# Optimization experiments

Measured on AMD Instinct MI355X. Metric: run time of the kernel, lower is better.

Reference implementation:

```python
import jax, jax.numpy as jnp
import numpy as np

B, S, D = 2, 2048, 2048
HQ, HKV, HD, HDV = 32, 8, 64, 64
QPK = HQ // HKV
EPS = 1e-5


def setup_inputs() -> dict:
    key = jax.random.key(0)
    ks = jax.random.split(key, 10)
    s = lambda fan_in: 1.0 / np.sqrt(fan_in)
    return {
        'x': jax.random.normal(ks[0], (B, S, D), dtype=jnp.float32),
        'ln_g': jnp.ones((D,), jnp.float32),
        'ln_b': jnp.zeros((D,), jnp.float32),
        'Wq': jax.random.uniform(ks[1], (D, HQ * HD), jnp.float32, -s(D), s(D)),
        'bq': jax.random.uniform(ks[2], (HQ * HD,), jnp.float32, -s(D), s(D)),
        'Wk': jax.random.uniform(ks[3], (D, HKV * HD), jnp.float32, -s(D), s(D)),
        'bk': jax.random.uniform(ks[4], (HKV * HD,), jnp.float32, -s(D), s(D)),
        'Wv': jax.random.uniform(ks[5], (D, HKV * HDV), jnp.float32, -s(D), s(D)),
        'bv': jax.random.uniform(ks[6], (HKV * HDV,), jnp.float32, -s(D), s(D)),
        'Wo': jax.random.uniform(ks[7], (HQ * HDV, D), jnp.float32, -s(HQ * HDV), s(HQ * HDV)),
        'bo': jax.random.uniform(ks[8], (D,), jnp.float32, -s(HQ * HDV), s(HQ * HDV)),
    }


def reference(x, ln_g, ln_b, Wq, bq, Wk, bk, Wv, bv, Wo, bo):
    # LayerNorm
    mu = jnp.mean(x, axis=-1, keepdims=True)
    var = jnp.mean(jnp.square(x - mu), axis=-1, keepdims=True)
    xn = (x - mu) * jax.lax.rsqrt(var + EPS) * ln_g + ln_b

    q = (xn @ Wq + bq).reshape(B, S, HKV, QPK, HD) * (1.0 / np.sqrt(HD))
    k = (xn @ Wk + bk).reshape(B, S, HKV, HD)
    v = (xn @ Wv + bv).reshape(B, S, HKV, HDV)

    # scores: (b, t=query, T=key, h, q_per_kv)
    scores = jnp.einsum('bthqd,bThd->btThq', q, k)
    # causal mask: -inf where T > t (upper triangle above diagonal)
    mask = jnp.triu(jnp.full((S, S), -jnp.inf, dtype=scores.dtype), 1)
    scores = scores + mask[None, :, :, None, None]
    # NOTE: source softmaxes over dim=-4, i.e. the QUERY axis t -> axis=1 here
    scores = jax.nn.softmax(scores, axis=1)
    out = jnp.einsum('btThq,bThd->bthqd', scores, v)
    out = out.reshape(B, S, HQ * HDV)
    return out @ Wo + bo
```

## Files before the change

kernel.cpp:

```cpp
#include <hip/hip_runtime.h>

#define Bb  2
#define Ss  2048
#define Dd  2048
#define HKV 8
#define QPK 4
#define HD  64
#define MR  (Bb * Ss)
#define NQ  2048
#define NKV 512

#define LOG2E 1.4426950408889634f

typedef unsigned short u16;
typedef unsigned int u32;
typedef __attribute__((ext_vector_type(8))) short s16x8;
typedef __attribute__((ext_vector_type(4))) float f32x4;

__device__ __forceinline__ u16 f2bf(float f) {
  unsigned u = __float_as_uint(f);
  u += 0x7fffu + ((u >> 16) & 1u);
  return (u16)(u >> 16);
}

__device__ __forceinline__ void gload16(const u16* g, u16* l) {
  __builtin_amdgcn_global_load_lds(
      (const __attribute__((address_space(1))) unsigned int*)g,
      (__attribute__((address_space(3))) unsigned int*)l, 16, 0, 0);
}

__device__ __forceinline__ u32 cvtpk_bf16(float a, float b) {
  u32 r;
  asm volatile("v_cvt_pk_bf16_f32 %0, %1, %2" : "=v"(r) : "v"(a), "v"(b));
  return r;
}

#define BAR()    asm volatile("s_barrier" ::: "memory")
#define WAITV4() asm volatile("s_waitcnt vmcnt(4)" ::: "memory")
#define WAITV2() asm volatile("s_waitcnt vmcnt(2)" ::: "memory")
#define WAITV0() asm volatile("s_waitcnt vmcnt(0)" ::: "memory")

__global__ __launch_bounds__(256) void ln_kernel(
    const float* __restrict__ x, const float* __restrict__ g,
    const float* __restrict__ be, u16* __restrict__ xn)
{
  int row = blockIdx.x;
  int tid = threadIdx.x;
  const float4* xr = (const float4*)(x + (size_t)row * Dd);
  float4 a = xr[tid];
  float4 b4 = xr[tid + 256];
  float s  = a.x + a.y + a.z + a.w + b4.x + b4.y + b4.z + b4.w;
  float ss = a.x*a.x + a.y*a.y + a.z*a.z + a.w*a.w
           + b4.x*b4.x + b4.y*b4.y + b4.z*b4.z + b4.w*b4.w;
  #pragma unroll
  for (int off = 32; off > 0; off >>= 1) {
    s  += __shfl_down(s, off);
    ss += __shfl_down(ss, off);
  }
  __shared__ float red[8];
  int lane = tid & 63, w = tid >> 6;
  if (lane == 0) { red[w] = s; red[4 + w] = ss; }
  __syncthreads();
  s  = red[0] + red[1] + red[2] + red[3];
  ss = red[4] + red[5] + red[6] + red[7];
  float mu = s * (1.0f / Dd);
  float rs = rsqrtf(ss * (1.0f / Dd) - mu * mu + 1e-5f);

  u16* xo = xn + (size_t)row * Dd;
  const float4* gv4 = (const float4*)g;
  const float4* bv4 = (const float4*)be;
  #pragma unroll
  for (int p = 0; p < 2; ++p) {
    int idx = tid + p * 256;
    float4 xv = (p == 0) ? a : b4;
    float4 gg = gv4[idx], bb = bv4[idx];
    ushort4 pk;
    pk.x = f2bf((xv.x - mu) * rs * gg.x + bb.x);
    pk.y = f2bf((xv.y - mu) * rs * gg.y + bb.y);
    pk.z = f2bf((xv.z - mu) * rs * gg.z + bb.z);
    pk.w = f2bf((xv.w - mu) * rs * gg.w + bb.w);
    *(ushort4*)(xo + idx * 4) = pk;
  }
}

__global__ __launch_bounds__(256) void transpose_cast(
    const float* __restrict__ W, u16* __restrict__ WT, int K, int N)
{
  __shared__ float tile[32][33];
  int tx = threadIdx.x & 31, ty = threadIdx.x >> 5;
  int n0 = blockIdx.x * 32, k0 = blockIdx.y * 32;
  #pragma unroll
  for (int i = 0; i < 4; ++i)
    tile[ty + 8 * i][tx] = W[(size_t)(k0 + ty + 8 * i) * N + n0 + tx];
  __syncthreads();
  #pragma unroll
  for (int i = 0; i < 4; ++i)
    WT[(size_t)(n0 + ty + 8 * i) * K + k0 + tx] = f2bf(tile[tx][ty + 8 * i]);
}

__global__ __launch_bounds__(256) void transpose_v(
    const u16* __restrict__ vb, u16* __restrict__ vT)
{
  __shared__ u16 tile[32][33];
  int tx = threadIdx.x & 31, ty = threadIdx.x >> 5;
  int c0 = blockIdx.x * 32;
  int r0 = blockIdx.y * 32;
  #pragma unroll
  for (int i = 0; i < 4; ++i)
    tile[ty + 8 * i][tx] = vb[(size_t)(r0 + ty + 8 * i) * NKV + c0 + tx];
  __syncthreads();
  int b = r0 >> 11, t = r0 & 2047;
  #pragma unroll
  for (int i = 0; i < 4; ++i)
    vT[((size_t)(b * NKV + c0 + ty + 8 * i)) * Ss + t + tx] = tile[tx][ty + 8 * i];
}

__device__ __forceinline__ void gemm8_core(
    const u16* __restrict__ A, const u16* __restrict__ BT, int K,
    int brow, int bcol, u16* __restrict__ As, u16* __restrict__ Bs,
    f32x4 (&acc)[8][4])
{
  const int tid  = threadIdx.x;
  const int lane = tid & 63;
  const int wave = tid >> 6;
  const int wr = wave >> 2, wc = wave & 3;
  const int m16 = lane & 15, quad = lane >> 4;
  const int NT = K >> 6;

  const int r0 = tid >> 3;
  const int sg = (tid & 7) ^ (r0 & 7);
  const u16* Asrc = A  + (size_t)(brow + r0) * K + sg * 8;
  const u16* Bsrc = BT + (size_t)(bcol + r0) * K + sg * 8;
  u16* AsW = As + wave * 512;
  u16* BsW = Bs + wave * 512;
  const size_t a64 = (size_t)64 * K;

  const int sl0 = (quad ^ (m16 & 7)) * 8;
  const int sl1 = ((quad | 4) ^ (m16 & 7)) * 8;
  const u16* Afr = As + wr * 8192 + m16 * 64;
  const u16* Bfr = Bs + (wc >> 1) * 8192 + ((wc & 1) * 64 + m16) * 64;

  #pragma unroll
  for (int h = 0; h < 2; ++h) {
    gload16(Asrc + (size_t)(h * 128) * K, AsW + h * 8192);
    gload16(Asrc + (size_t)(h * 128) * K + a64, AsW + h * 8192 + 4096);
    gload16(Bsrc + (size_t)(h * 128) * K, BsW + h * 8192);
    gload16(Bsrc + (size_t)(h * 128) * K + a64, BsW + h * 8192 + 4096);
  }
  #pragma unroll
  for (int h = 0; h < 2; ++h) {
    gload16(Bsrc + (size_t)(h * 128) * K + 64, BsW + 16384 + h * 8192);
    gload16(Bsrc + (size_t)(h * 128) * K + a64 + 64, BsW + 16384 + h * 8192 + 4096);
  }
  WAITV4();
  BAR();

  for (int t = 0; t < NT; ++t) {
    const int bi = t & 1;
    const u16* Abuf = Afr + bi * 16384;
    const u16* Bbuf = Bfr + bi * 16384;
    s16x8 bfr[4][2];
    #pragma unroll
    for (int ph = 0; ph < 4; ++ph) {
      s16x8 a0k0 = *(const s16x8*)(Abuf + (ph * 2 + 0) * 1024 + sl0);
      s16x8 a0k1 = *(const s16x8*)(Abuf + (ph * 2 + 0) * 1024 + sl1);
      s16x8 a1k0 = *(const s16x8*)(Abuf + (ph * 2 + 1) * 1024 + sl0);
      s16x8 a1k1 = *(const s16x8*)(Abuf + (ph * 2 + 1) * 1024 + sl1);
      if (ph == 0) {
        #pragma unroll
        for (int nj = 0; nj < 4; ++nj) {
          bfr[nj][0] = *(const s16x8*)(Bbuf + nj * 1024 + sl0);
          bfr[nj][1] = *(const s16x8*)(Bbuf + nj * 1024 + sl1);
        }
      }
      if (ph < 2) {
        if (t + 1 < NT) {
          const u16* g = Asrc + (size_t)(ph * 128) * K + (t + 1) * 64;
          u16* l = AsW + (bi ^ 1) * 16384 + ph * 8192;
          gload16(g, l);
          gload16(g + a64, l + 4096);
        }
      } else {
        if (t + 2 < NT) {
          const u16* g = Bsrc + (size_t)((ph - 2) * 128) * K + (t + 2) * 64;
          u16* l = BsW + bi * 16384 + (ph - 2) * 8192;
          gload16(g, l);
          gload16(g + a64, l + 4096);
        }
      }
      BAR();
      __builtin_amdgcn_s_setprio(1);
      #pragma unroll
      for (int nj = 0; nj < 4; ++nj) {
        acc[ph*2+0][nj] = __builtin_amdgcn_mfma_f32_16x16x32_bf16(a0k0, bfr[nj][0], acc[ph*2+0][nj], 0, 0, 0);
        acc[ph*2+0][nj] = __builtin_amdgcn_mfma_f32_16x16x32_bf16(a0k1, bfr[nj][1], acc[ph*2+0][nj], 0, 0, 0);
        acc[ph*2+1][nj] = __builtin_amdgcn_mfma_f32_16x16x32_bf16(a1k0, bfr[nj][0], acc[ph*2+1][nj], 0, 0, 0);
        acc[ph*2+1][nj] = __builtin_amdgcn_mfma_f32_16x16x32_bf16(a1k1, bfr[nj][1], acc[ph*2+1][nj], 0, 0, 0);
      }
      __builtin_amdgcn_s_setprio(0);
      if (ph == 3) {
        if (t + 2 < NT) WAITV4(); else WAITV0();
      }
      BAR();
    }
  }
}

__global__ __launch_bounds__(512) void gemm8_qkv(
    const u16* __restrict__ A, const u16* __restrict__ BT,
    const float* __restrict__ bq, const float* __restrict__ bk,
    const float* __restrict__ bv,
    u16* __restrict__ qb, u16* __restrict__ kb, u16* __restrict__ vb)
{
  __shared__ u16 As[32768];
  __shared__ u16 Bs[32768];
  int nbx = 12;
  int id  = blockIdx.y * nbx + blockIdx.x;
  int nwg = 192;
  int swz = (id & 7) * (nwg >> 3) + (id >> 3);
  int bx = swz % nbx, by = swz / nbx;

  f32x4 acc[8][4] = {};
  gemm8_core(A, BT, Dd, by * 256, bx * 256, As, Bs, acc);

  u16* outp; const float* bp; int ldo, cb; float scale;
  if (bx < 8)       { outp = qb; bp = bq; ldo = NQ;  cb = bx * 256;        scale = 0.125f * LOG2E; }
  else if (bx < 10) { outp = kb; bp = bk; ldo = NKV; cb = (bx - 8) * 256;  scale = 1.0f; }
  else              { outp = vb; bp = bv; ldo = NKV; cb = (bx - 10) * 256; scale = 1.0f; }

  int lane = threadIdx.x & 63, wave = threadIdx.x >> 6;
  int wr = wave >> 2, wc = wave & 3;
  int m16 = lane & 15, quad = lane >> 4;
  int colb = cb + (wc >> 1) * 128 + (wc & 1) * 64;
  #pragma unroll
  for (int nj = 0; nj < 4; ++nj) {
    int col = colb + nj * 16 + m16;
    float bc = bp[col];
    #pragma unroll
    for (int mi = 0; mi < 8; ++mi)
      #pragma unroll
      for (int rr = 0; rr < 4; ++rr) {
        int row = by * 256 + wr * 128 + mi * 16 + quad * 4 + rr;
        outp[(size_t)row * ldo + col] = f2bf((acc[mi][nj][rr] + bc) * scale);
      }
  }
}

__global__ __launch_bounds__(512) void gemm8_wo(
    const u16* __restrict__ A, const u16* __restrict__ BT,
    const float* __restrict__ bias, float* __restrict__ C, int N, int K)
{
  __shared__ u16 As[32768];
  __shared__ u16 Bs[16384];
  int nbx = N >> 7;
  int id  = blockIdx.y * nbx + blockIdx.x;
  int nwg = gridDim.x * gridDim.y;
  int swz = (id & 7) * (nwg >> 3) + (id >> 3);
  int bx = swz % nbx, by = swz / nbx;

  const int tid  = threadIdx.x;
  const int lane = tid & 63;
  const int wave = tid >> 6;
  const int wr = wave >> 2, wc = wave & 3;
  const int m16 = lane & 15, quad = lane >> 4;
  const int NT = K >> 6;

  const int r0 = tid >> 3;
  const int sg = (tid & 7) ^ (r0 & 7);
  const u16* Asrc = A  + (size_t)(by * 256 + r0) * K + sg * 8;
  const u16* Bsrc = BT + (size_t)(bx * 128 + r0) * K + sg * 8;
  u16* AsW = As + wave * 512;
  u16* BsW = Bs + wave * 512;
  const size_t a64 = (size_t)64 * K;

  const int sl0 = (quad ^ (m16 & 7)) * 8;
  const int sl1 = ((quad | 4) ^ (m16 & 7)) * 8;
  const u16* Afr = As + wr * 8192 + m16 * 64;
  const u16* Bfr = Bs + (wc * 32 + m16) * 64;

  f32x4 acc[8][2] = {};

  #pragma unroll
  for (int h = 0; h < 2; ++h) {
    gload16(Asrc + (size_t)(h * 128) * K, AsW + h * 8192);
    gload16(Asrc + (size_t)(h * 128) * K + a64, AsW + h * 8192 + 4096);
  }
  gload16(Bsrc, BsW);
  gload16(Bsrc + a64, BsW + 4096);
  gload16(Bsrc + 64, BsW + 8192);
  gload16(Bsrc + a64 + 64, BsW + 8192 + 4096);
  WAITV2();
  BAR();

  for (int t = 0; t < NT; ++t) {
    const int bi = t & 1;
    const u16* Abuf = Afr + bi * 16384;
    const u16* Bbuf = Bfr + bi * 8192;
    s16x8 bfr[2][2];
    #pragma unroll
    for (int ph = 0; ph < 4; ++ph) {
      s16x8 a0k0 = *(const s16x8*)(Abuf + (ph * 2 + 0) * 1024 + sl0);
      s16x8 a0k1 = *(const s16x8*)(Abuf + (ph * 2 + 0) * 1024 + sl1);
      s16x8 a1k0 = *(const s16x8*)(Abuf + (ph * 2 + 1) * 1024 + sl0);
      s16x8 a1k1 = *(const s16x8*)(Abuf + (ph * 2 + 1) * 1024 + sl1);
      if (ph == 0) {
        #pragma unroll
        for (int nj = 0; nj < 2; ++nj) {
          bfr[nj][0] = *(const s16x8*)(Bbuf + nj * 1024 + sl0);
          bfr[nj][1] = *(const s16x8*)(Bbuf + nj * 1024 + sl1);
        }
      }
      if (ph < 2) {
        if (t + 1 < NT) {
          const u16* g = Asrc + (size_t)(ph * 128) * K + (t + 1) * 64;
          u16* l = AsW + (bi ^ 1) * 16384 + ph * 8192;
          gload16(g, l);
          gload16(g + a64, l + 4096);
        }
      } else if (ph == 2) {
        if (t + 2 < NT) {
          const u16* g = Bsrc + (size_t)(t + 2) * 64;
          u16* l = BsW + bi * 8192;
          gload16(g, l);
          gload16(g + a64, l + 4096);
        }
      }
      BAR();
      __builtin_amdgcn_s_setprio(1);
      #pragma unroll
      for (int nj = 0; nj < 2; ++nj) {
        acc[ph*2+0][nj] = __builtin_amdgcn_mfma_f32_16x16x32_bf16(a0k0, bfr[nj][0], acc[ph*2+0][nj], 0, 0, 0);
        acc[ph*2+0][nj] = __builtin_amdgcn_mfma_f32_16x16x32_bf16(a0k1, bfr[nj][1], acc[ph*2+0][nj], 0, 0, 0);
        acc[ph*2+1][nj] = __builtin_amdgcn_mfma_f32_16x16x32_bf16(a1k0, bfr[nj][0], acc[ph*2+1][nj], 0, 0, 0);
        acc[ph*2+1][nj] = __builtin_amdgcn_mfma_f32_16x16x32_bf16(a1k1, bfr[nj][1], acc[ph*2+1][nj], 0, 0, 0);
      }
      __builtin_amdgcn_s_setprio(0);
      if (ph == 3) {
        if (t + 2 < NT) WAITV2(); else WAITV0();
      }
      BAR();
    }
  }

  int colb = bx * 128 + wc * 32;
  #pragma unroll
  for (int nj = 0; nj < 2; ++nj) {
    int col = colb + nj * 16 + m16;
    float bc = bias[col];
    #pragma unroll
    for (int mi = 0; mi < 8; ++mi)
      #pragma unroll
      for (int rr = 0; rr < 4; ++rr) {
        int row = by * 256 + wr * 128 + mi * 16 + quad * 4 + rr;
        C[(size_t)row * N + col] = acc[mi][nj][rr] + bc;
      }
  }
}

__global__ __launch_bounds__(256) void pass_a_mfma(
    const u16* __restrict__ qb, const u16* __restrict__ kb,
    float* __restrict__ cst)
{
  __shared__ u16 Qs[2][64 * 64];
  int combo = blockIdx.x;
  int qk = combo & 3, bh = combo >> 2;
  int b = bh >> 3, h = bh & 7;
  int g = blockIdx.y;
  int tid = threadIdx.x;
  int lane = tid & 63, wave = tid >> 6;
  int m16 = lane & 15, quad = lane >> 4;
  int T0w = g * 128 + wave * 32;

  const u16* kbase = kb + (size_t)b * Ss * NKV + h * HD;
  const u16* qbase = qb + (size_t)b * Ss * NQ + (h * QPK + qk) * HD;

  s16x8 kf[2][2];
  #pragma unroll
  for (int jg = 0; jg < 2; ++jg)
    #pragma unroll
    for (int dc = 0; dc < 2; ++dc)
      kf[jg][dc] = *(const s16x8*)(kbase + (size_t)(T0w + jg * 16 + m16) * NKV + dc * 32 + quad * 8);

  float ms[2] = {-1e30f, -1e30f};
  float ls[2] = {0.f, 0.f};
  int srow  = (wave << 3) + (lane >> 3);
  int slot0 = (lane & 7) ^ (lane >> 3);
  int sl0 = quad ^ (m16 & 7);
  int sl1 = (quad | 4) ^ (m16 & 7);
  int tDiag = T0w & ~63;

  {
    u16* QsW = &Qs[0][(wave * 8) * 64];
    int t0 = g * 128;
    gload16(qbase + (size_t)(t0 + srow) * NQ + slot0 * 8, QsW);
    gload16(qbase + (size_t)(t0 + srow + 32) * NQ + slot0 * 8, QsW + 32 * 64);
  }

  for (int t0 = g * 128; t0 < Ss; t0 += 64) {
    int cur = (t0 >> 6) & 1;
    bool nxt = (t0 + 64 < Ss);
    if (nxt) {
      u16* QsW = &Qs[cur ^ 1][(wave * 8) * 64];
      gload16(qbase + (size_t)(t0 + 64 + srow) * NQ + slot0 * 8, QsW);
      gload16(qbase + (size_t)(t0 + 64 + srow + 32) * NQ + slot0 * 8, QsW + 32 * 64);
      WAITV2();
    } else {
      WAITV0();
    }
    BAR();
    if (t0 + 63 < T0w) { BAR(); continue; }

    const u16* Qc = &Qs[cur][0];
    s16x8 af[4][2];
    #pragma unroll
    for (int i = 0; i < 4; ++i) {
      af[i][0] = *(const s16x8*)(Qc + (i * 16 + m16) * 64 + sl0 * 8);
      af[i][1] = *(const s16x8*)(Qc + (i * 16 + m16) * 64 + sl1 * 8);
    }
    f32x4 acc[4][2];
    #pragma unroll
    for (int i = 0; i < 4; ++i)
      #pragma unroll
      for (int jg = 0; jg < 2; ++jg) {
        f32x4 z = {};
        z = __builtin_amdgcn_mfma_f32_16x16x32_bf16(af[i][0], kf[jg][0], z, 0, 0, 0);
        acc[i][jg] = __builtin_amdgcn_mfma_f32_16x16x32_bf16(af[i][1], kf[jg][1], z, 0, 0, 0);
      }
    if (t0 == tDiag) {
      #pragma unroll
      for (int i = 0; i < 4; ++i)
        #pragma unroll
        for (int jg = 0; jg < 2; ++jg) {
          int tg = t0 + i * 16 + quad * 4;
          int Tg = T0w + jg * 16 + m16;
          #pragma unroll
          for (int r = 0; r < 4; ++r)
            if (tg + r < Tg) acc[i][jg][r] = -3e38f;
        }
    }
    #pragma unroll
    for (int jg = 0; jg < 2; ++jg) {
      float bm = -3e38f;
      #pragma unroll
      for (int i = 0; i < 4; ++i)
        #pragma unroll
        for (int r = 0; r < 4; ++r) bm = fmaxf(bm, acc[i][jg][r]);
      float mn = fmaxf(ms[jg], bm);
      float se = 0.f;
      #pragma unroll
      for (int i = 0; i < 4; ++i)
        #pragma unroll
        for (int r = 0; r < 4; ++r) se += exp2f(acc[i][jg][r] - mn);
      ls[jg] = ls[jg] * exp2f(ms[jg] - mn) + se;
      ms[jg] = mn;
    }
    BAR();
  }
  #pragma unroll
  for (int jg = 0; jg < 2; ++jg) {
    float m = ms[jg], l = ls[jg];
    #pragma unroll
    for (int off = 16; off <= 32; off <<= 1) {
      float mo = __shfl_xor(m, off);
      float lo = __shfl_xor(l, off);
      float mn = fmaxf(m, mo);
      l = l * exp2f(m - mn) + lo * exp2f(mo - mn);
      m = mn;
    }
    if (quad == 0)
      cst[(size_t)(bh * QPK + qk) * Ss + T0w + jg * 16 + m16] = m + __log2f(l);
  }
}

__global__ __launch_bounds__(256) void pass_b_mfma(
    const u16* __restrict__ qb, const u16* __restrict__ kb,
    const u16* __restrict__ vT, const float* __restrict__ cst,
    u16* __restrict__ attn)
{
  __shared__ u16 Ks[2][64 * 64];
  __shared__ u16 Vs[2][64 * 64];
  int combo = blockIdx.x;
  int qk = combo & 3, bh = combo >> 2;
  int b = bh >> 3, h = bh & 7;
  int g = 31 - blockIdx.y;
  int tid = threadIdx.x;
  int lane = tid & 63, wave = tid >> 6;
  int m16 = lane & 15, quad = lane >> 4;
  int trow = g * 64 + wave * 16;

  const u16* qbase = qb + (size_t)b * Ss * NQ + (h * QPK + qk) * HD;
  const u16* kbase = kb + (size_t)b * Ss * NKV + h * HD;
  const u16* vbase = vT + (size_t)(bh * 64) * Ss;
  const float* cbase = cst + (size_t)(bh * QPK + qk) * Ss;

  s16x8 qf[2];
  #pragma unroll
  for (int dc = 0; dc < 2; ++dc)
    qf[dc] = *(const s16x8*)(qbase + (size_t)(trow + m16) * NQ + dc * 32 + quad * 8);

  f32x4 oacc[4] = {};
  int srow  = (wave << 3) + (lane >> 3);
  int slot0 = (lane & 7) ^ (lane >> 3);
  int sl0 = quad ^ (m16 & 7);
  int sl1 = (quad | 4) ^ (m16 & 7);
  int Tend = g * 64;

  {
    u16* KsW = &Ks[0][(wave * 8) * 64];
    u16* VsW = &Vs[0][(wave * 8) * 64];
    gload16(kbase + (size_t)srow * NKV + slot0 * 8, KsW);
    gload16(kbase + (size_t)(srow + 32) * NKV + slot0 * 8, KsW + 32 * 64);
    gload16(vbase + (size_t)srow * Ss + slot0 * 8, VsW);
    gload16(vbase + (size_t)(srow + 32) * Ss + slot0 * 8, VsW + 32 * 64);
  }

  for (int T0 = 0; T0 <= Tend; T0 += 64) {
    int cur = (T0 >> 6) & 1;
    bool nxt = (T0 + 64 <= Tend);
    float4 cc[4];
    #pragma unroll
    for (int i = 0; i < 4; ++i)
      cc[i] = *(const float4*)(cbase + T0 + i * 16 + quad * 4);
    __builtin_amdgcn_sched_barrier(0);
    if (nxt) {
      u16* KsW = &Ks[cur ^ 1][(wave * 8) * 64];
      u16* VsW = &Vs[cur ^ 1][(wave * 8) * 64];
      gload16(kbase + (size_t)(T0 + 64 + srow) * NKV + slot0 * 8, KsW);
      gload16(kbase + (size_t)(T0 + 64 + srow + 32) * NKV + slot0 * 8, KsW + 32 * 64);
      gload16(vbase + (size_t)srow * Ss + T0 + 64 + slot0 * 8, VsW);
      gload16(vbase + (size_t)(srow + 32) * Ss + T0 + 64 + slot0 * 8, VsW + 32 * 64);
      WAITV4();
    } else {
      WAITV0();
    }
    BAR();
    bool diag = (T0 == Tend);
    const u16* Kc = &Ks[cur][0];
    const u16* Vc = &Vs[cur][0];
    #pragma unroll
    for (int tc = 0; tc < 2; ++tc) {
      u32 A[2], Bw[2];
      #pragma unroll
      for (int ii = 0; ii < 2; ++ii) {
        int i = tc * 2 + ii;
        s16x8 k0 = *(const s16x8*)(Kc + (i * 16 + m16) * 64 + sl0 * 8);
        s16x8 k1 = *(const s16x8*)(Kc + (i * 16 + m16) * 64 + sl1 * 8);
        f32x4 z = {};
        z = __builtin_amdgcn_mfma_f32_16x16x32_bf16(k0, qf[0], z, 0, 0, 0);
        z = __builtin_amdgcn_mfma_f32_16x16x32_bf16(k1, qf[1], z, 0, 0, 0);
        float4 c4 = cc[i];
        float w0 = exp2f(z[0] - c4.x);
        float w1 = exp2f(z[1] - c4.y);
        float w2 = exp2f(z[2] - c4.z);
        float w3 = exp2f(z[3] - c4.w);
        if (diag) {
          int t  = trow + m16;
          int Tg = T0 + i * 16 + quad * 4;
          if (Tg + 0 > t) w0 = 0.f;
          if (Tg + 1 > t) w1 = 0.f;
          if (Tg + 2 > t) w2 = 0.f;
          if (Tg + 3 > t) w3 = 0.f;
        }
        A[ii]  = cvtpk_bf16(w0, w1);
        Bw[ii] = cvtpk_bf16(w2, w3);
      }
      asm volatile("v_permlane32_swap_b32 %0, %1" : "+v"(A[0]),  "+v"(A[1]));
      asm volatile("v_permlane16_swap_b32 %0, %1" : "+v"(A[0]),  "+v"(A[1]));
      asm volatile("v_permlane32_swap_b32 %0, %1" : "+v"(Bw[0]), "+v"(Bw[1]));
      asm volatile("v_permlane16_swap_b32 %0, %1" : "+v"(Bw[0]), "+v"(Bw[1]));
      union { uint4 u; s16x8 v; } pu;
      pu.u.x = A[0]; pu.u.y = Bw[0]; pu.u.z = A[1]; pu.u.w = Bw[1];
      s16x8 pa = pu.v;
      #pragma unroll
      for (int dj = 0; dj < 4; ++dj) {
        int vsl = (quad | (tc << 2)) ^ (m16 & 7);
        s16x8 vf = *(const s16x8*)(Vc + (dj * 16 + m16) * 64 + vsl * 8);
        oacc[dj] = __builtin_amdgcn_mfma_f32_16x16x32_bf16(pa, vf, oacc[dj], 0, 0, 0);
      }
    }
    BAR();
  }
  u16* abase = attn + (size_t)b * Ss * NQ + (h * QPK + qk) * HD;
  #pragma unroll
  for (int dj = 0; dj < 4; ++dj)
    #pragma unroll
    for (int r = 0; r < 4; ++r)
      abase[(size_t)(trow + quad * 4 + r) * NQ + dj * 16 + m16] = f2bf(oacc[dj][r]);
}

extern "C" void kernel_launch(void* const* d_in, const int* in_sizes, int n_in,
                              void* d_out, int out_size, void* d_ws, size_t ws_size,
                              hipStream_t stream)
{
  (void)in_sizes; (void)n_in; (void)out_size; (void)ws_size;
  const float* x   = (const float*)d_in[0];
  const float* lng = (const float*)d_in[1];
  const float* lnb = (const float*)d_in[2];
  const float* Wq  = (const float*)d_in[3];
  const float* bq  = (const float*)d_in[4];
  const float* Wk  = (const float*)d_in[5];
  const float* bk  = (const float*)d_in[6];
  const float* Wv  = (const float*)d_in[7];
  const float* bv  = (const float*)d_in[8];
  const float* Wo  = (const float*)d_in[9];
  const float* bo  = (const float*)d_in[10];
  float* out = (float*)d_out;

  char* ws = (char*)d_ws;
  size_t off = 0;
  auto take = [&](size_t bytes) -> char* {
    char* p = ws + off;
    off += (bytes + 255) & ~(size_t)255;
    return p;
  };
  u16*    xnb   = (u16*)take((size_t)MR * Dd * 2);
  u16*    wqkvT = (u16*)take((size_t)(NQ + 2 * NKV) * Dd * 2);
  u16*    woT   = (u16*)take((size_t)Dd * NQ * 2);
  u16*    qbB   = (u16*)take((size_t)MR * NQ * 2);
  u16*    kbB   = (u16*)take((size_t)MR * NKV * 2);
  u16*    vbB   = (u16*)take((size_t)MR * NKV * 2);
  u16*    vTb   = (u16*)take((size_t)MR * NKV * 2);
  float*  cst   = (float*)take((size_t)Bb * HKV * QPK * Ss * 4);
  u16*    attnb = (u16*)take((size_t)MR * NQ * 2);

  ln_kernel<<<MR, 256, 0, stream>>>(x, lng, lnb, xnb);
  transpose_cast<<<dim3(NQ / 32, Dd / 32), 256, 0, stream>>>(Wq, wqkvT, Dd, NQ);
  transpose_cast<<<dim3(NKV / 32, Dd / 32), 256, 0, stream>>>(Wk, wqkvT + (size_t)NQ * Dd, Dd, NKV);
  transpose_cast<<<dim3(NKV / 32, Dd / 32), 256, 0, stream>>>(Wv, wqkvT + (size_t)(NQ + NKV) * Dd, Dd, NKV);
  transpose_cast<<<dim3(NQ / 32, Dd / 32), 256, 0, stream>>>(Wo, woT, Dd, NQ);

  gemm8_qkv<<<dim3(12, 16), 512, 0, stream>>>(xnb, wqkvT, bq, bk, bv, qbB, kbB, vbB);
  transpose_v<<<dim3(NKV / 32, MR / 32), 256, 0, stream>>>(vbB, vTb);

  pass_a_mfma<<<dim3(64, 16), 256, 0, stream>>>(qbB, kbB, cst);
  pass_b_mfma<<<dim3(64, 32), 256, 0, stream>>>(qbB, kbB, vTb, cst, attnb);

  gemm8_wo<<<dim3(16, 16), 512, 0, stream>>>(attnb, woT, bo, out, Dd, NQ);
}
```

Baseline: 386.8 us.

## Triple-buffer GEMM pipeline, fuse V transpose into QKV epilogue, fold softmax offset

Replaces the 256x256 double-buffered QKV GEMM and the Wo GEMM with a shared 256x128 tile core that keeps three LDS stages in flight, prefetching two k-steps ahead. The QKV grid doubles to 384 workgroups. The V output is written directly in transposed layout from the GEMM epilogue, which removes the separate transpose kernel and its intermediate buffer. Pass A now stores the negated log-sum-exp so pass B can seed the MFMA accumulator with it and drop a subtraction per score. The cost is more LDS per workgroup, which may lower occupancy, and uncoalesced 8-byte strided stores for V.

```diff
diff --git a/kernel.cpp b/kernel.cpp
--- a/kernel.cpp
+++ b/kernel.cpp
@@ -36,6 +36,7 @@
 }
 
 #define BAR()    asm volatile("s_barrier" ::: "memory")
+#define WAITV6() asm volatile("s_waitcnt vmcnt(6)" ::: "memory")
 #define WAITV4() asm volatile("s_waitcnt vmcnt(4)" ::: "memory")
 #define WAITV2() asm volatile("s_waitcnt vmcnt(2)" ::: "memory")
 #define WAITV0() asm volatile("s_waitcnt vmcnt(0)" ::: "memory")
@@ -98,27 +99,10 @@
     WT[(size_t)(n0 + ty + 8 * i) * K + k0 + tx] = f2bf(tile[tx][ty + 8 * i]);
 }
 
-__global__ __launch_bounds__(256) void transpose_v(
-    const u16* __restrict__ vb, u16* __restrict__ vT)
-{
-  __shared__ u16 tile[32][33];
-  int tx = threadIdx.x & 31, ty = threadIdx.x >> 5;
-  int c0 = blockIdx.x * 32;
-  int r0 = blockIdx.y * 32;
-  #pragma unroll
-  for (int i = 0; i < 4; ++i)
-    tile[ty + 8 * i][tx] = vb[(size_t)(r0 + ty + 8 * i) * NKV + c0 + tx];
-  __syncthreads();
-  int b = r0 >> 11, t = r0 & 2047;
-  #pragma unroll
-  for (int i = 0; i < 4; ++i)
-    vT[((size_t)(b * NKV + c0 + ty + 8 * i)) * Ss + t + tx] = tile[tx][ty + 8 * i];
-}
-
-__device__ __forceinline__ void gemm8_core(
+__device__ __forceinline__ void gemm3_core(
     const u16* __restrict__ A, const u16* __restrict__ BT, int K,
     int brow, int bcol, u16* __restrict__ As, u16* __restrict__ Bs,
-    f32x4 (&acc)[8][4])
+    f32x4 (&acc)[8][2])
 {
   const int tid  = threadIdx.x;
   const int lane = tid & 63;
@@ -134,168 +118,38 @@
   u16* AsW = As + wave * 512;
   u16* BsW = Bs + wave * 512;
   const size_t a64 = (size_t)64 * K;
-
-  const int sl0 = (quad ^ (m16 & 7)) * 8;
-  const int sl1 = ((quad | 4) ^ (m16 & 7)) * 8;
-  const u16* Afr = As + wr * 8192 + m16 * 64;
-  const u16* Bfr = Bs + (wc >> 1) * 8192 + ((wc & 1) * 64 + m16) * 64;
-
-  #pragma unroll
-  for (int h = 0; h < 2; ++h) {
-    gload16(Asrc + (size_t)(h * 128) * K, AsW + h * 8192);
-    gload16(Asrc + (size_t)(h * 128) * K + a64, AsW + h * 8192 + 4096);
-    gload16(Bsrc + (size_t)(h * 128) * K, BsW + h * 8192);
-    gload16(Bsrc + (size_t)(h * 128) * K + a64, BsW + h * 8192 + 4096);
-  }
-  #pragma unroll
-  for (int h = 0; h < 2; ++h) {
-    gload16(Bsrc + (size_t)(h * 128) * K + 64, BsW + 16384 + h * 8192);
-    gload16(Bsrc + (size_t)(h * 128) * K + a64 + 64, BsW + 16384 + h * 8192 + 4096);
-  }
-  WAITV4();
-  BAR();
-
-  for (int t = 0; t < NT; ++t) {
-    const int bi = t & 1;
-    const u16* Abuf = Afr + bi * 16384;
-    const u16* Bbuf = Bfr + bi * 16384;
-    s16x8 bfr[4][2];
-    #pragma unroll
-    for (int ph = 0; ph < 4; ++ph) {
-      s16x8 a0k0 = *(const s16x8*)(Abuf + (ph * 2 + 0) * 1024 + sl0);
-      s16x8 a0k1 = *(const s16x8*)(Abuf + (ph * 2 + 0) * 1024 + sl1);
-      s16x8 a1k0 = *(const s16x8*)(Abuf + (ph * 2 + 1) * 1024 + sl0);
-      s16x8 a1k1 = *(const s16x8*)(Abuf + (ph * 2 + 1) * 1024 + sl1);
-      if (ph == 0) {
-        #pragma unroll
-        for (int nj = 0; nj < 4; ++nj) {
-          bfr[nj][0] = *(const s16x8*)(Bbuf + nj * 1024 + sl0);
-          bfr[nj][1] = *(const s16x8*)(Bbuf + nj * 1024 + sl1);
-        }
-      }
-      if (ph < 2) {
-        if (t + 1 < NT) {
-          const u16* g = Asrc + (size_t)(ph * 128) * K + (t + 1) * 64;
-          u16* l = AsW + (bi ^ 1) * 16384 + ph * 8192;
-          gload16(g, l);
-          gload16(g + a64, l + 4096);
-        }
-      } else {
-        if (t + 2 < NT) {
-          const u16* g = Bsrc + (size_t)((ph - 2) * 128) * K + (t + 2) * 64;
-          u16* l = BsW + bi * 16384 + (ph - 2) * 8192;
-          gload16(g, l);
-          gload16(g + a64, l + 4096);
-        }
-      }
-      BAR();
-      __builtin_amdgcn_s_setprio(1);
-      #pragma unroll
-      for (int nj = 0; nj < 4; ++nj) {
-        acc[ph*2+0][nj] = __builtin_amdgcn_mfma_f32_16x16x32_bf16(a0k0, bfr[nj][0], acc[ph*2+0][nj], 0, 0, 0);
-        acc[ph*2+0][nj] = __builtin_amdgcn_mfma_f32_16x16x32_bf16(a0k1, bfr[nj][1], acc[ph*2+0][nj], 0, 0, 0);
-        acc[ph*2+1][nj] = __builtin_amdgcn_mfma_f32_16x16x32_bf16(a1k0, bfr[nj][0], acc[ph*2+1][nj], 0, 0, 0);
-        acc[ph*2+1][nj] = __builtin_amdgcn_mfma_f32_16x16x32_bf16(a1k1, bfr[nj][1], acc[ph*2+1][nj], 0, 0, 0);
-      }
-      __builtin_amdgcn_s_setprio(0);
-      if (ph == 3) {
-        if (t + 2 < NT) WAITV4(); else WAITV0();
-      }
-      BAR();
-    }
-  }
-}
-
-__global__ __launch_bounds__(512) void gemm8_qkv(
-    const u16* __restrict__ A, const u16* __restrict__ BT,
-    const float* __restrict__ bq, const float* __restrict__ bk,
-    const float* __restrict__ bv,
-    u16* __restrict__ qb, u16* __restrict__ kb, u16* __restrict__ vb)
-{
-  __shared__ u16 As[32768];
-  __shared__ u16 Bs[32768];
-  int nbx = 12;
-  int id  = blockIdx.y * nbx + blockIdx.x;
-  int nwg = 192;
-  int swz = (id & 7) * (nwg >> 3) + (id >> 3);
-  int bx = swz % nbx, by = swz / nbx;
-
-  f32x4 acc[8][4] = {};
-  gemm8_core(A, BT, Dd, by * 256, bx * 256, As, Bs, acc);
-
-  u16* outp; const float* bp; int ldo, cb; float scale;
-  if (bx < 8)       { outp = qb; bp = bq; ldo = NQ;  cb = bx * 256;        scale = 0.125f * LOG2E; }
-  else if (bx < 10) { outp = kb; bp = bk; ldo = NKV; cb = (bx - 8) * 256;  scale = 1.0f; }
-  else              { outp = vb; bp = bv; ldo = NKV; cb = (bx - 10) * 256; scale = 1.0f; }
-
-  int lane = threadIdx.x & 63, wave = threadIdx.x >> 6;
-  int wr = wave >> 2, wc = wave & 3;
-  int m16 = lane & 15, quad = lane >> 4;
-  int colb = cb + (wc >> 1) * 128 + (wc & 1) * 64;
-  #pragma unroll
-  for (int nj = 0; nj < 4; ++nj) {
-    int col = colb + nj * 16 + m16;
-    float bc = bp[col];
-    #pragma unroll
-    for (int mi = 0; mi < 8; ++mi)
-      #pragma unroll
-      for (int rr = 0; rr < 4; ++rr) {
-        int row = by * 256 + wr * 128 + mi * 16 + quad * 4 + rr;
-        outp[(size_t)row * ldo + col] = f2bf((acc[mi][nj][rr] + bc) * scale);
-      }
-  }
-}
-
-__global__ __launch_bounds__(512) void gemm8_wo(
-    const u16* __restrict__ A, const u16* __restrict__ BT,
-    const float* __restrict__ bias, float* __restrict__ C, int N, int K)
-{
-  __shared__ u16 As[32768];
-  __shared__ u16 Bs[16384];
-  int nbx = N >> 7;
-  int id  = blockIdx.y * nbx + blockIdx.x;
-  int nwg = gridDim.x * gridDim.y;
-  int swz = (id & 7) * (nwg >> 3) + (id >> 3);
-  int bx = swz % nbx, by = swz / nbx;
-
-  const int tid  = threadIdx.x;
-  const int lane = tid & 63;
-  const int wave = tid >> 6;
-  const int wr = wave >> 2, wc = wave & 3;
-  const int m16 = lane & 15, quad = lane >> 4;
-  const int NT = K >> 6;
-
-  const int r0 = tid >> 3;
-  const int sg = (tid & 7) ^ (r0 & 7);
-  const u16* Asrc = A  + (size_t)(by * 256 + r0) * K + sg * 8;
-  const u16* Bsrc = BT + (size_t)(bx * 128 + r0) * K + sg * 8;
-  u16* AsW = As + wave * 512;
-  u16* BsW = Bs + wave * 512;
-  const size_t a64 = (size_t)64 * K;
+  const size_t a128 = (size_t)128 * K;
 
   const int sl0 = (quad ^ (m16 & 7)) * 8;
   const int sl1 = ((quad | 4) ^ (m16 & 7)) * 8;
   const u16* Afr = As + wr * 8192 + m16 * 64;
   const u16* Bfr = Bs + (wc * 32 + m16) * 64;
 
-  f32x4 acc[8][2] = {};
-
   #pragma unroll
   for (int h = 0; h < 2; ++h) {
-    gload16(Asrc + (size_t)(h * 128) * K, AsW + h * 8192);
-    gload16(Asrc + (size_t)(h * 128) * K + a64, AsW + h * 8192 + 4096);
+    gload16(Asrc + h * a128, AsW + h * 8192);
+    gload16(Asrc + h * a128 + a64, AsW + h * 8192 + 4096);
   }
   gload16(Bsrc, BsW);
   gload16(Bsrc + a64, BsW + 4096);
+  #pragma unroll
+  for (int h = 0; h < 2; ++h) {
+    gload16(Asrc + h * a128 + 64, AsW + 16384 + h * 8192);
+    gload16(Asrc + h * a128 + a64 + 64, AsW + 16384 + h * 8192 + 4096);
+  }
   gload16(Bsrc + 64, BsW + 8192);
   gload16(Bsrc + a64 + 64, BsW + 8192 + 4096);
-  WAITV2();
+  WAITV6();
   BAR();
 
   for (int t = 0; t < NT; ++t) {
-    const int bi = t & 1;
+    const int bi = t % 3;
+    const int bn = (t + 2) % 3;
     const u16* Abuf = Afr + bi * 16384;
     const u16* Bbuf = Bfr + bi * 8192;
+    const bool st = (t + 2 < NT);
+    const u16* Ag2 = Asrc + (size_t)(t + 2) * 64;
+    const u16* Bg2 = Bsrc + (size_t)(t + 2) * 64;
     s16x8 bfr[2][2];
     #pragma unroll
     for (int ph = 0; ph < 4; ++ph) {
@@ -310,19 +164,16 @@
           bfr[nj][1] = *(const s16x8*)(Bbuf + nj * 1024 + sl1);
         }
       }
-      if (ph < 2) {
-        if (t + 1 < NT) {
-          const u16* g = Asrc + (size_t)(ph * 128) * K + (t + 1) * 64;
-          u16* l = AsW + (bi ^ 1) * 16384 + ph * 8192;
-          gload16(g, l);
-          gload16(g + a64, l + 4096);
-        }
-      } else if (ph == 2) {
-        if (t + 2 < NT) {
-          const u16* g = Bsrc + (size_t)(t + 2) * 64;
-          u16* l = BsW + bi * 8192;
-          gload16(g, l);
-          gload16(g + a64, l + 4096);
+      if (st) {
+        if (ph == 0) {
+          gload16(Ag2, AsW + bn * 16384);
+          gload16(Ag2 + a64, AsW + bn * 16384 + 4096);
+        } else if (ph == 1) {
+          gload16(Ag2 + a128, AsW + bn * 16384 + 8192);
+          gload16(Ag2 + a128 + a64, AsW + bn * 16384 + 8192 + 4096);
+        } else if (ph == 2) {
+          gload16(Bg2, BsW + bn * 8192);
+          gload16(Bg2 + a64, BsW + bn * 8192 + 4096);
         }
       }
       BAR();
@@ -336,12 +187,101 @@
       }
       __builtin_amdgcn_s_setprio(0);
       if (ph == 3) {
-        if (t + 2 < NT) WAITV2(); else WAITV0();
+        if (st) WAITV6(); else WAITV0();
       }
       BAR();
     }
   }
-
+}
+
+__global__ __launch_bounds__(512) void gemm3_qkv(
+    const u16* __restrict__ A, const u16* __restrict__ BT,
+    const float* __restrict__ bq, const float* __restrict__ bk,
+    const float* __restrict__ bv,
+    u16* __restrict__ qb, u16* __restrict__ kb, u16* __restrict__ vT)
+{
+  __shared__ u16 As[3 * 16384];
+  __shared__ u16 Bs[3 * 8192];
+  int nbx = 24;
+  int id  = blockIdx.y * nbx + blockIdx.x;
+  int nwg = 384;
+  int swz = (id & 7) * (nwg >> 3) + (id >> 3);
+  int bx = swz % nbx, by = swz / nbx;
+
+  f32x4 acc[8][2] = {};
+  gemm3_core(A, BT, Dd, by * 256, bx * 128, As, Bs, acc);
+
+  int lane = threadIdx.x & 63, wave = threadIdx.x >> 6;
+  int wr = wave >> 2, wc = wave & 3;
+  int m16 = lane & 15, quad = lane >> 4;
+
+  if (bx < 16) {
+    int colb = bx * 128 + wc * 32;
+    #pragma unroll
+    for (int nj = 0; nj < 2; ++nj) {
+      int col = colb + nj * 16 + m16;
+      float bc = bq[col];
+      #pragma unroll
+      for (int mi = 0; mi < 8; ++mi)
+        #pragma unroll
+        for (int rr = 0; rr < 4; ++rr) {
+          int row = by * 256 + wr * 128 + mi * 16 + quad * 4 + rr;
+          qb[(size_t)row * NQ + col] = f2bf((acc[mi][nj][rr] + bc) * (0.125f * LOG2E));
+        }
+    }
+  } else if (bx < 20) {
+    int colb = (bx - 16) * 128 + wc * 32;
+    #pragma unroll
+    for (int nj = 0; nj < 2; ++nj) {
+      int col = colb + nj * 16 + m16;
+      float bc = bk[col];
+      #pragma unroll
+      for (int mi = 0; mi < 8; ++mi)
+        #pragma unroll
+        for (int rr = 0; rr < 4; ++rr) {
+          int row = by * 256 + wr * 128 + mi * 16 + quad * 4 + rr;
+          kb[(size_t)row * NKV + col] = f2bf(acc[mi][nj][rr] + bc);
+        }
+    }
+  } else {
+    int colb = (bx - 20) * 128 + wc * 32;
+    #pragma unroll
+    for (int nj = 0; nj < 2; ++nj) {
+      int col = colb + nj * 16 + m16;
+      float bc = bv[col];
+      #pragma unroll
+      for (int mi = 0; mi < 8; ++mi) {
+        int row = by * 256 + wr * 128 + mi * 16 + quad * 4;
+        int b = row >> 11, t = row & 2047;
+        ushort4 pk;
+        pk.x = f2bf(acc[mi][nj][0] + bc);
+        pk.y = f2bf(acc[mi][nj][1] + bc);
+        pk.z = f2bf(acc[mi][nj][2] + bc);
+        pk.w = f2bf(acc[mi][nj][3] + bc);
+        *(ushort4*)(vT + ((size_t)(b * NKV + col)) * Ss + t) = pk;
+      }
+    }
+  }
+}
+
+__global__ __launch_bounds__(512) void gemm3_wo(
+    const u16* __restrict__ A, const u16* __restrict__ BT,
+    const float* __restrict__ bias, float* __restrict__ C, int N, int K)
+{
+  __shared__ u16 As[3 * 16384];
+  __shared__ u16 Bs[3 * 8192];
+  int nbx = N >> 7;
+  int id  = blockIdx.y * nbx + blockIdx.x;
+  int nwg = gridDim.x * gridDim.y;
+  int swz = (id & 7) * (nwg >> 3) + (id >> 3);
+  int bx = swz % nbx, by = swz / nbx;
+
+  f32x4 acc[8][2] = {};
+  gemm3_core(A, BT, K, by * 256, bx * 128, As, Bs, acc);
+
+  int lane = threadIdx.x & 63, wave = threadIdx.x >> 6;
+  int wr = wave >> 2, wc = wave & 3;
+  int m16 = lane & 15, quad = lane >> 4;
   int colb = bx * 128 + wc * 32;
   #pragma unroll
   for (int nj = 0; nj < 2; ++nj) {
@@ -468,7 +408,7 @@
       m = mn;
     }
     if (quad == 0)
-      cst[(size_t)(bh * QPK + qk) * Ss + T0w + jg * 16 + m16] = m + __log2f(l);
+      cst[(size_t)(bh * QPK + qk) * Ss + T0w + jg * 16 + m16] = -(m + __log2f(l));
   }
 }
 
@@ -545,14 +485,14 @@
         int i = tc * 2 + ii;
         s16x8 k0 = *(const s16x8*)(Kc + (i * 16 + m16) * 64 + sl0 * 8);
         s16x8 k1 = *(const s16x8*)(Kc + (i * 16 + m16) * 64 + sl1 * 8);
-        f32x4 z = {};
+        float4 c4 = cc[i];
+        f32x4 z = {c4.x, c4.y, c4.z, c4.w};
         z = __builtin_amdgcn_mfma_f32_16x16x32_bf16(k0, qf[0], z, 0, 0, 0);
         z = __builtin_amdgcn_mfma_f32_16x16x32_bf16(k1, qf[1], z, 0, 0, 0);
-        float4 c4 = cc[i];
-        float w0 = exp2f(z[0] - c4.x);
-        float w1 = exp2f(z[1] - c4.y);
-        float w2 = exp2f(z[2] - c4.z);
-        float w3 = exp2f(z[3] - c4.w);
+        float w0 = exp2f(z[0]);
+        float w1 = exp2f(z[1]);
+        float w2 = exp2f(z[2]);
+        float w3 = exp2f(z[3]);
         if (diag) {
           int t  = trow + m16;
           int Tg = T0 + i * 16 + quad * 4;
@@ -618,7 +558,6 @@
   u16*    woT   = (u16*)take((size_t)Dd * NQ * 2);
   u16*    qbB   = (u16*)take((size_t)MR * NQ * 2);
   u16*    kbB   = (u16*)take((size_t)MR * NKV * 2);
-  u16*    vbB   = (u16*)take((size_t)MR * NKV * 2);
   u16*    vTb   = (u16*)take((size_t)MR * NKV * 2);
   float*  cst   = (float*)take((size_t)Bb * HKV * QPK * Ss * 4);
   u16*    attnb = (u16*)take((size_t)MR * NQ * 2);
@@ -629,11 +568,10 @@
   transpose_cast<<<dim3(NKV / 32, Dd / 32), 256, 0, stream>>>(Wv, wqkvT + (size_t)(NQ + NKV) * Dd, Dd, NKV);
   transpose_cast<<<dim3(NQ / 32, Dd / 32), 256, 0, stream>>>(Wo, woT, Dd, NQ);
 
-  gemm8_qkv<<<dim3(12, 16), 512, 0, stream>>>(xnb, wqkvT, bq, bk, bv, qbB, kbB, vbB);
-  transpose_v<<<dim3(NKV / 32, MR / 32), 256, 0, stream>>>(vbB, vTb);
+  gemm3_qkv<<<dim3(24, 16), 512, 0, stream>>>(xnb, wqkvT, bq, bk, bv, qbB, kbB, vTb);
 
   pass_a_mfma<<<dim3(64, 16), 256, 0, stream>>>(qbB, kbB, cst);
   pass_b_mfma<<<dim3(64, 32), 256, 0, stream>>>(qbB, kbB, vTb, cst, attnb);
 
-  gemm8_wo<<<dim3(16, 16), 512, 0, stream>>>(attnb, woT, bo, out, Dd, NQ);
-}
+  gemm3_wo<<<dim3(16, 16), 512, 0, stream>>>(attnb, woT, bo, out, Dd, NQ);
+}
```

New measurement: 394.8 us. 1.02x slower.

## Merge weight transposes, write V transposed from QKV GEMM, fold softmax constant

Applied to the files above, without the earlier changes.

The four weight transpose-cast launches become one kernel that picks its source matrix from the block index. The QKV GEMM epilogue now writes V directly in transposed layout, which removes the separate transpose_v kernel and its intermediate buffer. Pass A stores the negated log-sum-exp so pass B can seed the MFMA accumulator with it and skip a subtraction before each exp2. The transposed V stores are 8-byte writes strided by the sequence length, which may coalesce worse than the row-major stores they replace.

```diff
diff --git a/kernel.cpp b/kernel.cpp
--- a/kernel.cpp
+++ b/kernel.cpp
@@ -83,36 +83,29 @@
   }
 }
 
-__global__ __launch_bounds__(256) void transpose_cast(
-    const float* __restrict__ W, u16* __restrict__ WT, int K, int N)
-{
+__global__ __launch_bounds__(256) void transpose_all(
+    const float* __restrict__ Wq, const float* __restrict__ Wk,
+    const float* __restrict__ Wv, const float* __restrict__ Wo,
+    u16* __restrict__ wqkvT, u16* __restrict__ woT)
+{
+  int id = blockIdx.x;
+  const float* W; u16* WT; int N, loc;
+  if (id < 4096)      { W = Wq; WT = wqkvT;                          N = NQ;  loc = id; }
+  else if (id < 5120) { W = Wk; WT = wqkvT + (size_t)NQ * Dd;        N = NKV; loc = id - 4096; }
+  else if (id < 6144) { W = Wv; WT = wqkvT + (size_t)(NQ + NKV) * Dd; N = NKV; loc = id - 5120; }
+  else                { W = Wo; WT = woT;                            N = NQ;  loc = id - 6144; }
+  int nx = N >> 5;
+  int n0 = (loc % nx) * 32, k0 = (loc / nx) * 32;
+
   __shared__ float tile[32][33];
   int tx = threadIdx.x & 31, ty = threadIdx.x >> 5;
-  int n0 = blockIdx.x * 32, k0 = blockIdx.y * 32;
   #pragma unroll
   for (int i = 0; i < 4; ++i)
     tile[ty + 8 * i][tx] = W[(size_t)(k0 + ty + 8 * i) * N + n0 + tx];
   __syncthreads();
   #pragma unroll
   for (int i = 0; i < 4; ++i)
-    WT[(size_t)(n0 + ty + 8 * i) * K + k0 + tx] = f2bf(tile[tx][ty + 8 * i]);
-}
-
-__global__ __launch_bounds__(256) void transpose_v(
-    const u16* __restrict__ vb, u16* __restrict__ vT)
-{
-  __shared__ u16 tile[32][33];
-  int tx = threadIdx.x & 31, ty = threadIdx.x >> 5;
-  int c0 = blockIdx.x * 32;
-  int r0 = blockIdx.y * 32;
-  #pragma unroll
-  for (int i = 0; i < 4; ++i)
-    tile[ty + 8 * i][tx] = vb[(size_t)(r0 + ty + 8 * i) * NKV + c0 + tx];
-  __syncthreads();
-  int b = r0 >> 11, t = r0 & 2047;
-  #pragma unroll
-  for (int i = 0; i < 4; ++i)
-    vT[((size_t)(b * NKV + c0 + ty + 8 * i)) * Ss + t + tx] = tile[tx][ty + 8 * i];
+    WT[(size_t)(n0 + ty + 8 * i) * Dd + k0 + tx] = f2bf(tile[tx][ty + 8 * i]);
 }
 
 __device__ __forceinline__ void gemm8_core(
@@ -210,7 +203,7 @@
     const u16* __restrict__ A, const u16* __restrict__ BT,
     const float* __restrict__ bq, const float* __restrict__ bk,
     const float* __restrict__ bv,
-    u16* __restrict__ qb, u16* __restrict__ kb, u16* __restrict__ vb)
+    u16* __restrict__ qb, u16* __restrict__ kb, u16* __restrict__ vT)
 {
   __shared__ u16 As[32768];
   __shared__ u16 Bs[32768];
@@ -223,26 +216,57 @@
   f32x4 acc[8][4] = {};
   gemm8_core(A, BT, Dd, by * 256, bx * 256, As, Bs, acc);
 
-  u16* outp; const float* bp; int ldo, cb; float scale;
-  if (bx < 8)       { outp = qb; bp = bq; ldo = NQ;  cb = bx * 256;        scale = 0.125f * LOG2E; }
-  else if (bx < 10) { outp = kb; bp = bk; ldo = NKV; cb = (bx - 8) * 256;  scale = 1.0f; }
-  else              { outp = vb; bp = bv; ldo = NKV; cb = (bx - 10) * 256; scale = 1.0f; }
-
   int lane = threadIdx.x & 63, wave = threadIdx.x >> 6;
   int wr = wave >> 2, wc = wave & 3;
   int m16 = lane & 15, quad = lane >> 4;
-  int colb = cb + (wc >> 1) * 128 + (wc & 1) * 64;
-  #pragma unroll
-  for (int nj = 0; nj < 4; ++nj) {
-    int col = colb + nj * 16 + m16;
-    float bc = bp[col];
-    #pragma unroll
-    for (int mi = 0; mi < 8; ++mi)
-      #pragma unroll
-      for (int rr = 0; rr < 4; ++rr) {
-        int row = by * 256 + wr * 128 + mi * 16 + quad * 4 + rr;
-        outp[(size_t)row * ldo + col] = f2bf((acc[mi][nj][rr] + bc) * scale);
-      }
+  int wcol = (wc >> 1) * 128 + (wc & 1) * 64;
+
+  if (bx < 8) {
+    int colb = bx * 256 + wcol;
+    #pragma unroll
+    for (int nj = 0; nj < 4; ++nj) {
+      int col = colb + nj * 16 + m16;
+      float bc = bq[col];
+      #pragma unroll
+      for (int mi = 0; mi < 8; ++mi)
+        #pragma unroll
+        for (int rr = 0; rr < 4; ++rr) {
+          int row = by * 256 + wr * 128 + mi * 16 + quad * 4 + rr;
+          qb[(size_t)row * NQ + col] = f2bf((acc[mi][nj][rr] + bc) * (0.125f * LOG2E));
+        }
+    }
+  } else if (bx < 10) {
+    int colb = (bx - 8) * 256 + wcol;
+    #pragma unroll
+    for (int nj = 0; nj < 4; ++nj) {
+      int col = colb + nj * 16 + m16;
+      float bc = bk[col];
+      #pragma unroll
+      for (int mi = 0; mi < 8; ++mi)
+        #pragma unroll
+        for (int rr = 0; rr < 4; ++rr) {
+          int row = by * 256 + wr * 128 + mi * 16 + quad * 4 + rr;
+          kb[(size_t)row * NKV + col] = f2bf(acc[mi][nj][rr] + bc);
+        }
+    }
+  } else {
+    int colb = (bx - 10) * 256 + wcol;
+    #pragma unroll
+    for (int nj = 0; nj < 4; ++nj) {
+      int col = colb + nj * 16 + m16;
+      float bc = bv[col];
+      #pragma unroll
+      for (int mi = 0; mi < 8; ++mi) {
+        int row = by * 256 + wr * 128 + mi * 16 + quad * 4;
+        int b = row >> 11, t = row & 2047;
+        ushort4 pk;
+        pk.x = f2bf(acc[mi][nj][0] + bc);
+        pk.y = f2bf(acc[mi][nj][1] + bc);
+        pk.z = f2bf(acc[mi][nj][2] + bc);
+        pk.w = f2bf(acc[mi][nj][3] + bc);
+        *(ushort4*)(vT + ((size_t)(b * NKV + col)) * Ss + t) = pk;
+      }
+    }
   }
 }
 
@@ -468,7 +492,7 @@
       m = mn;
     }
     if (quad == 0)
-      cst[(size_t)(bh * QPK + qk) * Ss + T0w + jg * 16 + m16] = m + __log2f(l);
+      cst[(size_t)(bh * QPK + qk) * Ss + T0w + jg * 16 + m16] = -(m + __log2f(l));
   }
 }
 
@@ -545,14 +569,14 @@
         int i = tc * 2 + ii;
         s16x8 k0 = *(const s16x8*)(Kc + (i * 16 + m16) * 64 + sl0 * 8);
         s16x8 k1 = *(const s16x8*)(Kc + (i * 16 + m16) * 64 + sl1 * 8);
-        f32x4 z = {};
+        float4 c4 = cc[i];
+        f32x4 z = {c4.x, c4.y, c4.z, c4.w};
         z = __builtin_amdgcn_mfma_f32_16x16x32_bf16(k0, qf[0], z, 0, 0, 0);
         z = __builtin_amdgcn_mfma_f32_16x16x32_bf16(k1, qf[1], z, 0, 0, 0);
-        float4 c4 = cc[i];
-        float w0 = exp2f(z[0] - c4.x);
-        float w1 = exp2f(z[1] - c4.y);
-        float w2 = exp2f(z[2] - c4.z);
-        float w3 = exp2f(z[3] - c4.w);
+        float w0 = exp2f(z[0]);
+        float w1 = exp2f(z[1]);
+        float w2 = exp2f(z[2]);
+        float w3 = exp2f(z[3]);
         if (diag) {
           int t  = trow + m16;
           int Tg = T0 + i * 16 + quad * 4;
@@ -618,19 +642,14 @@
   u16*    woT   = (u16*)take((size_t)Dd * NQ * 2);
   u16*    qbB   = (u16*)take((size_t)MR * NQ * 2);
   u16*    kbB   = (u16*)take((size_t)MR * NKV * 2);
-  u16*    vbB   = (u16*)take((size_t)MR * NKV * 2);
   u16*    vTb   = (u16*)take((size_t)MR * NKV * 2);
   float*  cst   = (float*)take((size_t)Bb * HKV * QPK * Ss * 4);
   u16*    attnb = (u16*)take((size_t)MR * NQ * 2);
 
   ln_kernel<<<MR, 256, 0, stream>>>(x, lng, lnb, xnb);
-  transpose_cast<<<dim3(NQ / 32, Dd / 32), 256, 0, stream>>>(Wq, wqkvT, Dd, NQ);
-  transpose_cast<<<dim3(NKV / 32, Dd / 32), 256, 0, stream>>>(Wk, wqkvT + (size_t)NQ * Dd, Dd, NKV);
-  transpose_cast<<<dim3(NKV / 32, Dd / 32), 256, 0, stream>>>(Wv, wqkvT + (size_t)(NQ + NKV) * Dd, Dd, NKV);
-  transpose_cast<<<dim3(NQ / 32, Dd / 32), 256, 0, stream>>>(Wo, woT, Dd, NQ);
-
-  gemm8_qkv<<<dim3(12, 16), 512, 0, stream>>>(xnb, wqkvT, bq, bk, bv, qbB, kbB, vbB);
-  transpose_v<<<dim3(NKV / 32, MR / 32), 256, 0, stream>>>(vbB, vTb);
+  transpose_all<<<10240, 256, 0, stream>>>(Wq, Wk, Wv, Wo, wqkvT, woT);
+
+  gemm8_qkv<<<dim3(12, 16), 512, 0, stream>>>(xnb, wqkvT, bq, bk, bv, qbB, kbB, vTb);
 
   pass_a_mfma<<<dim3(64, 16), 256, 0, stream>>>(qbB, kbB, cst);
   pass_b_mfma<<<dim3(64, 32), 256, 0, stream>>>(qbB, kbB, vTb, cst, attnb);
```

New measurement: 382.0 us. About the same (-1.2%).
